# Performance work log

Measured on AMD Instinct MI355X. Metric: run time of the kernel, lower is better.

Reference implementation:

```python
import jax, jax.numpy as jnp
import numpy as np

NUM_EMOTIONS = 8
EMOTION_DIM = 32
MAX_EMOTIONS = 3
HIDDEN = 768
NUM_HEADS = 8
HEAD_DIM = HIDDEN // NUM_HEADS // 2  # 48
DEPTH = 0
LAMBDA_INIT = 0.8 - 0.6 * float(np.exp(-0.3 * DEPTH))  # 0.2
EPS = 1e-5


def setup_inputs() -> dict:
    key = jax.random.key(0)
    ks = jax.random.split(key, 16)
    B = 16384
    emotion_indices = jax.random.randint(ks[0], (B, MAX_EMOTIONS), 0, NUM_EMOTIONS)
    confidence_values = jax.random.uniform(ks[1], (B, MAX_EMOTIONS), dtype=jnp.float32)
    emb_table = jax.random.normal(ks[2], (NUM_EMOTIONS + 1, EMOTION_DIM), jnp.float32)
    emb_table = emb_table.at[NUM_EMOTIONS].set(0.0)  # padding_idx row
    s1 = 1.0 / np.sqrt(EMOTION_DIM)
    s2 = 1.0 / np.sqrt(HIDDEN)
    W1 = jax.random.normal(ks[3], (EMOTION_DIM, HIDDEN), jnp.float32) * s1
    b1 = jnp.zeros((HIDDEN,), jnp.float32)
    ln_g = jnp.ones((HIDDEN,), jnp.float32)
    ln_b = jnp.zeros((HIDDEN,), jnp.float32)
    Wq = jax.random.normal(ks[4], (HIDDEN, HIDDEN), jnp.float32) * s2
    Wk = jax.random.normal(ks[5], (HIDDEN, HIDDEN), jnp.float32) * s2
    Wv = jax.random.normal(ks[6], (HIDDEN, HIDDEN), jnp.float32) * s2
    Wo = jax.random.normal(ks[7], (HIDDEN, HIDDEN), jnp.float32) * s2
    lq1 = jax.random.normal(ks[8], (HEAD_DIM,), jnp.float32) * 0.1
    lk1 = jax.random.normal(ks[9], (HEAD_DIM,), jnp.float32) * 0.1
    lq2 = jax.random.normal(ks[10], (HEAD_DIM,), jnp.float32) * 0.1
    lk2 = jax.random.normal(ks[11], (HEAD_DIM,), jnp.float32) * 0.1
    subln_w = jnp.ones((2 * HEAD_DIM,), jnp.float32)
    return dict(emotion_indices=emotion_indices, confidence_values=confidence_values,
                emb_table=emb_table, W1=W1, b1=b1, ln_g=ln_g, ln_b=ln_b,
                Wq=Wq, Wk=Wk, Wv=Wv, Wo=Wo,
                lq1=lq1, lk1=lk1, lq2=lq2, lk2=lk2, subln_w=subln_w)


def _rotary_tables(seq_len, dim):
    inv_freq = 1.0 / (10000.0 ** (jnp.arange(0, dim, 2, dtype=jnp.float32) / dim))  # [dim/2]
    t = jnp.arange(seq_len, dtype=jnp.float32)
    ang = jnp.outer(t, inv_freq)  # [S, dim/2]
    return jnp.cos(ang), jnp.sin(ang)


def _apply_rope(x, cos, sin):
    # x: [B, S, H, D]; cos/sin: [S, D/2] (interleaved pairs)
    x1, x2 = x[..., 0::2], x[..., 1::2]
    c = cos[None, :, None, :]
    s = sin[None, :, None, :]
    r1 = x1 * c - x2 * s
    r2 = x1 * s + x2 * c
    return jnp.stack([r1, r2], axis=-1).reshape(x.shape)


def _forward(emotion_indices, confidence_values, emb_table, W1, b1, ln_g, ln_b,
             Wq, Wk, Wv, Wo, lq1, lk1, lq2, lk2, subln_w):
    B, S = emotion_indices.shape  # S == MAX_EMOTIONS
    idx = jnp.where(emotion_indices < 0, NUM_EMOTIONS, emotion_indices)

    # embedding lookup + confidence weighting
    emb = emb_table[idx] * confidence_values[..., None]  # [B,S,32]

    # Linear + LayerNorm + GELU (dropout = identity in eval)
    h = emb @ W1 + b1  # [B,S,768]
    mu = jnp.mean(h, axis=-1, keepdims=True)
    var = jnp.mean(jnp.square(h - mu), axis=-1, keepdims=True)
    h = (h - mu) / jnp.sqrt(var + EPS) * ln_g + ln_b
    h = jax.nn.gelu(h, approximate=False)

    # rotary tables
    cos, sin = _rotary_tables(S, HEAD_DIM)

    # additive attention mask: -inf over padded key columns
    pad = (idx == NUM_EMOTIONS)  # [B,S]
    neg_inf = jnp.asarray(-jnp.inf, h.dtype)
    mask = jnp.where(pad[:, None, None, :], neg_inf, 0.0)  # [B,1,1,S] -> bcast to [B,1,S,S]

    # differential attention
    q = (h @ Wq).reshape(B, S, 2 * NUM_HEADS, HEAD_DIM)
    k = (h @ Wk).reshape(B, S, 2 * NUM_HEADS, HEAD_DIM)
    v = (h @ Wv).reshape(B, S, NUM_HEADS, 2 * HEAD_DIM)
    q = _apply_rope(q, cos, sin)
    k = _apply_rope(k, cos, sin)

    scale = HEAD_DIM ** -0.5
    scores = jnp.einsum('bqhd,bkhd->bhqk', q, k) * scale + mask  # [B,2H,S,S]
    attn = jax.nn.softmax(scores, axis=-1)
    attn = attn.reshape(B, NUM_HEADS, 2, S, S)
    lam = (jnp.exp(jnp.sum(lq1 * lk1)) - jnp.exp(jnp.sum(lq2 * lk2)) + LAMBDA_INIT)
    diff = attn[:, :, 0] - lam * attn[:, :, 1]  # [B,H,S,S]

    out = jnp.einsum('bhqk,bkhd->bqhd', diff, v)  # [B,S,H,2d]
    # sublayer RMSNorm over last dim
    rms = jnp.sqrt(jnp.mean(jnp.square(out), axis=-1, keepdims=True) + EPS)
    out = out / rms * subln_w
    out = out * (1.0 - LAMBDA_INIT)
    out = out.reshape(B, S, HIDDEN) @ Wo  # [B,S,768]

    # masked mean pooling over non-padding positions
    npad = (~pad).astype(out.dtype)[..., None]  # [B,S,1]
    summed = jnp.sum(out * npad, axis=1)
    denom = jnp.maximum(jnp.sum(npad, axis=1), 1.0)
    return summed / denom  # [B,768]


def reference(emotion_indices, confidence_values, emb_table, W1, b1, ln_g, ln_b,
              Wq, Wk, Wv, Wo, lq1, lk1, lq2, lk2, subln_w):
    return _forward(emotion_indices, confidence_values, emb_table, W1, b1, ln_g, ln_b,
                    Wq, Wk, Wv, Wo, lq1, lk1, lq2, lk2, subln_w)
```

## Files before the change

### kernel.cpp

```cpp
#include <hip/hip_runtime.h>
#include <hip/hip_bf16.h>
#include <math.h>
#include <stdint.h>

typedef __hip_bfloat16 bf16;
typedef __attribute__((ext_vector_type(8))) short short8;
typedef __attribute__((ext_vector_type(4))) float f32x4;
typedef __attribute__((ext_vector_type(2))) unsigned int u32x2;

#define NB 16384
#define HID 768
#define EPS_LN 1e-5f
#define LAM_INIT 0.2f

__device__ __forceinline__ float bf2f(bf16 x){ return __bfloat162float(x); }
__device__ __forceinline__ bf16  f2bf(float x){ return __float2bfloat16(x); }
__device__ __forceinline__ float bfbits(uint32_t lo16){ return __uint_as_float(lo16 << 16); }
__device__ __forceinline__ uint32_t f2bfbits(float x){
  union { float f; uint32_t u; } v; v.f = x;
  uint32_t u = v.u;
  uint32_t r = (u + 0x7fff + ((u >> 16) & 1)) >> 16;
  return r;
}

template<typename T> __device__ __forceinline__ float ldv(const void* p, int i);
template<> __device__ __forceinline__ float ldv<float>(const void* p, int i){ return ((const float*)p)[i]; }
template<> __device__ __forceinline__ float ldv<bf16 >(const void* p, int i){ return bf2f(((const bf16*)p)[i]); }

template<typename T> __device__ __forceinline__ void stv(T* p, float v);
template<> __device__ __forceinline__ void stv<float>(float* p, float v){ *p = v; }
template<> __device__ __forceinline__ void stv<bf16 >(bf16*  p, float v){ *p = f2bf(v); }

__device__ __forceinline__ void async_copy16(void* lds, const void* g){
  __builtin_amdgcn_global_load_lds(
      (const __attribute__((address_space(1))) unsigned int*)g,
      (__attribute__((address_space(3))) unsigned int*)lds, 16, 0, 0);
}

__device__ __forceinline__ float wred64(float v){
  #pragma unroll
  for (int m = 1; m <= 32; m <<= 1) v += __shfl_xor(v, m, 64);
  return v;
}

__global__ void prep_kernel(const void* etab, const void* lq1, const void* lk1,
                            const void* lq2, const void* lk2, float* prep){
  const int lane = threadIdx.x;
  const uint32_t* p = (const uint32_t*)((const char*)etab + 512);
  int v = (lane < 16) ? (int)p[lane] : 0;
  #pragma unroll
  for (int m = 1; m <= 32; m <<= 1) v |= __shfl_xor(v, m, 64);
  const int isbf = (v == 0) ? 1 : 0;
  if (lane == 0) ((int*)prep)[0] = isbf;

  float p1 = 0.f, p2 = 0.f;
  if (lane < 48){
    if (isbf){ p1 = ldv<bf16>(lq1,lane)*ldv<bf16>(lk1,lane); p2 = ldv<bf16>(lq2,lane)*ldv<bf16>(lk2,lane); }
    else     { p1 = ldv<float>(lq1,lane)*ldv<float>(lk1,lane); p2 = ldv<float>(lq2,lane)*ldv<float>(lk2,lane); }
  }
  p1 = wred64(p1); p2 = wred64(p2);
  if (lane == 0) prep[1] = expf(p1) - expf(p2) + LAM_INIT;

  if (lane < 24){
    float invf = powf(10000.f, -(float)(2*lane)/48.f);
    #pragma unroll
    for (int s=0;s<3;++s){
      float ang = (float)s*invf;
      float c = cosf(ang), sv = sinf(ang);
      prep[16  + s*32 + lane] = c;
      prep[128 + s*32 + lane] = sv;
      prep[256 + (s*24 + lane)*2    ] = c;
      prep[256 + (s*24 + lane)*2 + 1] = sv;
    }
  }
}

template<typename T>
__device__ __forceinline__ void transpose_body(bf16 (*tile)[33], const void* src, bf16* dst){
  const int n0 = blockIdx.x*32, k0 = blockIdx.y*32;
  const int tx = threadIdx.x, ty = threadIdx.y;
  #pragma unroll
  for (int r=0;r<4;++r)
    tile[ty + 8*r][tx] = f2bf(ldv<T>(src, (k0 + ty + 8*r)*HID + n0 + tx));
  __syncthreads();
  #pragma unroll
  for (int r=0;r<4;++r)
    dst[(size_t)(n0 + ty + 8*r)*HID + k0 + tx] = tile[tx][ty + 8*r];
}

__global__ __launch_bounds__(256) void transpose_weights(
    const void* Wq, const void* Wk, const void* Wv, const void* Wo,
    bf16* __restrict__ WqkvT, bf16* __restrict__ WoT, const float* prep)
{
  __shared__ bf16 tile[32][33];
  const int z = blockIdx.z;
  const void* src = (z==0)? Wq : (z==1)? Wk : (z==2)? Wv : Wo;
  bf16* dst = (z<3)? (WqkvT + (size_t)z*HID*HID) : WoT;
  if (((const int*)prep)[0]) transpose_body<bf16 >(tile, src, dst);
  else                       transpose_body<float>(tile, src, dst);
}

template<typename T>
__device__ __forceinline__ void embed_body(
    float (*s_emb)[32], float (*s_h)[HID],
    const int* eidx, const void* conf, const void* etab, const void* W1,
    const void* b1, const void* lng, const void* lnb, bf16* hout, int tok0)
{
  const int tid = threadIdx.x;
  const int tl0 = blockIdx.x * 16;

  for (int i = tid; i < 16*32; i += 256) {
    int t = i >> 5, e = i & 31;
    int tt = tok0 + tl0 + t;
    int id = eidx[tt]; if (id < 0) id = 8;
    float cf = ldv<T>(conf, tt);
    s_emb[t][e] = ldv<T>(etab, id*32 + e) * cf;
  }
  __syncthreads();

  float acc0[16], acc1[16], acc2[16];
  #pragma unroll
  for (int t=0;t<16;++t){ acc0[t]=0.f; acc1[t]=0.f; acc2[t]=0.f; }
  const int c0 = tid, c1 = tid+256, c2 = tid+512;
  #pragma unroll 4
  for (int e=0;e<32;++e){
    float w0 = ldv<T>(W1, e*HID+c0), w1 = ldv<T>(W1, e*HID+c1), w2 = ldv<T>(W1, e*HID+c2);
    #pragma unroll
    for (int t=0;t<16;++t){
      float em = s_emb[t][e];
      acc0[t] += em*w0; acc1[t] += em*w1; acc2[t] += em*w2;
    }
  }
  float bb0 = ldv<T>(b1,c0), bb1 = ldv<T>(b1,c1), bb2 = ldv<T>(b1,c2);
  #pragma unroll
  for (int t=0;t<16;++t){
    s_h[t][c0] = acc0[t]+bb0; s_h[t][c1] = acc1[t]+bb1; s_h[t][c2] = acc2[t]+bb2;
  }
  __syncthreads();

  const int wv = tid>>6, lane = tid&63;
  for (int t = wv; t < 16; t += 4) {
    float x[12]; float sm = 0.f, sq = 0.f;
    #pragma unroll
    for (int j=0;j<12;++j){ float xv = s_h[t][lane + 64*j]; x[j]=xv; sm += xv; sq += xv*xv; }
    sm = wred64(sm); sq = wred64(sq);
    float mu  = sm * (1.f/768.f);
    float var = sq * (1.f/768.f) - mu*mu;
    float rs  = rsqrtf(fmaxf(var, 0.f) + EPS_LN);
    #pragma unroll
    for (int j=0;j<12;++j){
      int col = lane + 64*j;
      float y  = (x[j]-mu)*rs*ldv<T>(lng,col) + ldv<T>(lnb,col);
      float ge = 0.5f*y*(1.f + erff(y*0.70710678118f));
      hout[(size_t)(tl0+t)*HID + col] = f2bf(ge);
    }
  }
}

__global__ __launch_bounds__(256) void embed_fc1_ln_gelu(
    const int* __restrict__ eidx, const void* conf, const void* etab,
    const void* W1, const void* b1, const void* lng, const void* lnb,
    bf16* __restrict__ hout, int tok0, const float* prep)
{
  __shared__ float s_emb[16][32];
  __shared__ float s_h[16][HID];
  if (((const int*)prep)[0]) embed_body<bf16 >(s_emb, s_h, eidx, conf, etab, W1, b1, lng, lnb, hout, tok0);
  else                       embed_body<float>(s_emb, s_h, eidx, conf, etab, W1, b1, lng, lnb, hout, tok0);
}

template<typename OutT>
__device__ __forceinline__ void gemm_body(
    bf16* sA, bf16* sB,
    const bf16* __restrict__ A, const bf16* __restrict__ Bt, OutT* __restrict__ C,
    int K, int lda, int ldb, int ldc, int MT, int NT)
{
  int bid = blockIdx.x;
  int mt, nt;
  if ((MT & 7) == 0) {
    int x = bid & 7, j = bid >> 3;
    nt = j % NT;
    mt = x * (MT >> 3) + j / NT;
  } else { nt = bid % NT; mt = bid / NT; }

  const int tid = threadIdx.x;
  const int wave = tid >> 6, lane = tid & 63;
  const int m0 = mt * 128, n0 = nt * 128;
  const int wm = wave >> 1, wn = wave & 1;

  f32x4 acc[4][4];
  #pragma unroll
  for (int i=0;i<4;++i)
    #pragma unroll
    for (int j=0;j<4;++j) acc[i][j] = (f32x4){0.f,0.f,0.f,0.f};

  const char* Ag = (const char*)(A  + (size_t)m0 * lda);
  const char* Bg = (const char*)(Bt + (size_t)n0 * ldb);
  const int r8  = lane >> 3;
  const int cBx = ((lane & 7) ^ r8) * 16;

  #define STAGE(buf, kt) do {                                                   \
    _Pragma("unroll")                                                           \
    for (int ii = 0; ii < 4; ++ii) {                                            \
      const int i_ = wave*4 + ii;                                               \
      const int row_ = i_*8 + r8;                                               \
      async_copy16((char*)sA + (buf)*16384 + i_*1024 + lane*16,                 \
                   Ag + ((size_t)row_*lda + (kt))*2 + cBx);                     \
      async_copy16((char*)sB + (buf)*16384 + i_*1024 + lane*16,                 \
                   Bg + ((size_t)row_*ldb + (kt))*2 + cBx);                     \
    }                                                                           \
  } while(0)

  STAGE(0, 0);
  int cur = 0;
  const int rxor = (lane & 7) << 3;
  for (int kt = 0; kt < K; kt += 64) {
    __syncthreads();
    if (kt + 64 < K) STAGE(cur^1, kt + 64);
    const bf16* pA = sA + cur*8192;
    const bf16* pB = sB + cur*8192;
    #pragma unroll
    for (int ks = 0; ks < 64; ks += 32) {
      const int kq = (ks + (lane >> 4)*8) ^ rxor;
      short8 af[4], bfv[4];
      #pragma unroll
      for (int i=0;i<4;++i)
        af[i]  = *(const short8*)&pA[(wm*64 + i*16 + (lane&15))*64 + kq];
      #pragma unroll
      for (int j=0;j<4;++j)
        bfv[j] = *(const short8*)&pB[(wn*64 + j*16 + (lane&15))*64 + kq];
      #pragma unroll
      for (int i=0;i<4;++i)
        #pragma unroll
        for (int j=0;j<4;++j)
          acc[i][j] = __builtin_amdgcn_mfma_f32_16x16x32_bf16(af[i], bfv[j], acc[i][j], 0,0,0);
    }
    cur ^= 1;
  }
  #undef STAGE

  const int rb = (lane>>4)*4, cb = lane & 15;
  #pragma unroll
  for (int i=0;i<4;++i)
    #pragma unroll
    for (int r=0;r<4;++r) {
      const int grow = m0 + wm*64 + i*16 + rb + r;
      OutT* Cp = C + (size_t)grow*ldc + n0 + wn*64 + cb;
      #pragma unroll
      for (int j=0;j<4;++j) stv<OutT>(Cp + j*16, acc[i][j][r]);
    }
}

__global__ __launch_bounds__(256) void gemm_int(
    const bf16* __restrict__ A, const bf16* __restrict__ Bt, bf16* __restrict__ C,
    int K, int lda, int ldb, int ldc, int MT, int NT)
{
  __shared__ __align__(16) bf16 sA[2*128*64];
  __shared__ __align__(16) bf16 sB[2*128*64];
  gemm_body<bf16>(sA, sB, A, Bt, C, K, lda, ldb, ldc, MT, NT);
}

__global__ __launch_bounds__(256) void gemm_final(
    const bf16* __restrict__ A, const bf16* __restrict__ Bt, void* C,
    int K, int lda, int ldb, int ldc, int MT, int NT, const float* prep)
{
  __shared__ __align__(16) bf16 sA[2*128*64];
  __shared__ __align__(16) bf16 sB[2*128*64];
  if (((const int*)prep)[0]) gemm_body<bf16 >(sA, sB, A, Bt, (bf16*)C,  K, lda, ldb, ldc, MT, NT);
  else                       gemm_body<float>(sA, sB, A, Bt, (float*)C, K, lda, ldb, ldc, MT, NT);
}

template<typename T>
__device__ __forceinline__ void attn_body(
    const bf16* __restrict__ qkv, const int* __restrict__ eidx,
    const void* subw, bf16* __restrict__ obar, int b0, const float* prep)
{
  const int bl = blockIdx.x*4 + (threadIdx.x>>6);
  const int bg = b0 + bl;
  const int lane = threadIdx.x & 63;
  const int h  = lane >> 3;
  const int u  = lane & 7;
  const int g  = u >> 2;
  const int qd = u & 3;

  float npad[3];
  #pragma unroll
  for (int s=0;s<3;++s){ int id = eidx[bg*3+s]; npad[s] = (id < 0 || id == 8) ? 0.f : 1.f; }
  float denom = npad[0]+npad[1]+npad[2]; if (denom < 1.f) denom = 1.f;
  const float lam = prep[1];
  const float2* pk = (const float2*)(prep + 256);

  const char* base = (const char*)(qkv + (size_t)bl*3*2304);
  const int qoff = (2*h+g)*48 + qd*12;

  u32x2 qw[3][3], kw[3][3];
  #pragma unroll
  for (int s=0;s<3;++s){
    const char* qp = base + (size_t)(s*2304 + qoff)*2;
    const char* kp = qp + 768*2;
    #pragma unroll
    for (int t=0;t<3;++t){
      qw[s][t] = *(const u32x2*)(qp + t*8);
      kw[s][t] = *(const u32x2*)(kp + t*8);
    }
  }

  float sc[3][3];
  #pragma unroll
  for (int a=0;a<3;++a){ sc[a][0]=0.f; sc[a][1]=0.f; sc[a][2]=0.f; }
  #pragma unroll
  for (int j=0;j<6;++j){
    float qr1[3], qr2[3], kr1[3], kr2[3];
    #pragma unroll
    for (int s=0;s<3;++s){
      float2 cs = pk[s*24 + qd*6 + j];
      uint32_t qu = qw[s][j>>1][j&1], ku = kw[s][j>>1][j&1];
      float q1 = bfbits(qu & 0xffffu), q2 = bfbits(qu >> 16);
      float k1 = bfbits(ku & 0xffffu), k2 = bfbits(ku >> 16);
      qr1[s] = q1*cs.x - q2*cs.y;  qr2[s] = q1*cs.y + q2*cs.x;
      kr1[s] = k1*cs.x - k2*cs.y;  kr2[s] = k1*cs.y + k2*cs.x;
    }
    #pragma unroll
    for (int a=0;a<3;++a)
      #pragma unroll
      for (int b=0;b<3;++b) sc[a][b] += qr1[a]*kr1[b] + qr2[a]*kr2[b];
  }
  #pragma unroll
  for (int a=0;a<3;++a)
    #pragma unroll
    for (int b=0;b<3;++b){
      float v = sc[a][b];
      v += __shfl_xor(v, 1, 64);
      v += __shfl_xor(v, 2, 64);
      sc[a][b] = v;
    }

  const float scale = 0.14433756729740643f;
  float att[3][3];
  #pragma unroll
  for (int a=0;a<3;++a){
    float s0 = sc[a][0]*scale + (npad[0] > 0.f ? 0.f : -1e30f);
    float s1 = sc[a][1]*scale + (npad[1] > 0.f ? 0.f : -1e30f);
    float s2 = sc[a][2]*scale + (npad[2] > 0.f ? 0.f : -1e30f);
    float mx = fmaxf(s0, fmaxf(s1, s2));
    float e0 = expf(s0-mx), e1 = expf(s1-mx), e2 = expf(s2-mx);
    float inv = 1.f/(e0+e1+e2);
    att[a][0]=e0*inv; att[a][1]=e1*inv; att[a][2]=e2*inv;
  }
  float diff[3][3];
  #pragma unroll
  for (int a=0;a<3;++a)
    #pragma unroll
    for (int b=0;b<3;++b){
      float other = __shfl_xor(att[a][b], 4, 64);
      diff[a][b] = (g==0) ? (att[a][b] - lam*other) : (other - lam*att[a][b]);
    }

  const int vd = u*12;
  float vv[3][12];
  #pragma unroll
  for (int s=0;s<3;++s){
    const char* vp = base + (size_t)(s*2304 + 1536 + h*96 + vd)*2;
    #pragma unroll
    for (int t=0;t<3;++t){
      u32x2 w = *(const u32x2*)(vp + t*8);
      vv[s][t*4+0] = bfbits(w[0] & 0xffffu);
      vv[s][t*4+1] = bfbits(w[0] >> 16);
      vv[s][t*4+2] = bfbits(w[1] & 0xffffu);
      vv[s][t*4+3] = bfbits(w[1] >> 16);
    }
  }
  float sw[12];
  #pragma unroll
  for (int d=0;d<12;++d) sw[d] = ldv<T>(subw, vd + d);

  float acc[12];
  #pragma unroll
  for (int d=0;d<12;++d) acc[d] = 0.f;
  #pragma unroll
  for (int a=0;a<3;++a){
    float o[12]; float ss = 0.f;
    #pragma unroll
    for (int d=0;d<12;++d){
      o[d] = diff[a][0]*vv[0][d] + diff[a][1]*vv[1][d] + diff[a][2]*vv[2][d];
      ss += o[d]*o[d];
    }
    ss += __shfl_xor(ss, 1, 64);
    ss += __shfl_xor(ss, 2, 64);
    ss += __shfl_xor(ss, 4, 64);
    float rms = sqrtf(ss*(1.f/96.f) + 1e-5f);
    float kk  = npad[a]*0.8f/rms;
    #pragma unroll
    for (int d=0;d<12;++d) acc[d] += o[d]*kk*sw[d];
  }
  const float idn = 1.f/denom;
  char* op = (char*)obar + (size_t)(bg*HID + h*96 + vd)*2;
  #pragma unroll
  for (int t=0;t<3;++t){
    u32x2 w;
    w[0] = f2bfbits(acc[t*4+0]*idn) | (f2bfbits(acc[t*4+1]*idn) << 16);
    w[1] = f2bfbits(acc[t*4+2]*idn) | (f2bfbits(acc[t*4+3]*idn) << 16);
    *(u32x2*)(op + t*8) = w;
  }
}

__global__ __launch_bounds__(256) void attn_kernel(
    const bf16* __restrict__ qkv, const int* __restrict__ eidx,
    const void* subw, bf16* __restrict__ obar, int b0, const float* prep)
{
  if (((const int*)prep)[0]) attn_body<bf16 >(qkv, eidx, subw, obar, b0, prep);
  else                       attn_body<float>(qkv, eidx, subw, obar, b0, prep);
}

extern "C" void kernel_launch(void* const* d_in, const int* in_sizes, int n_in,
                              void* d_out, int out_size, void* d_ws, size_t ws_size,
                              hipStream_t stream)
{
  const int*  eidx = (const int*) d_in[0];
  const void* conf = d_in[1];
  const void* etab = d_in[2];
  const void* W1   = d_in[3];
  const void* b1   = d_in[4];
  const void* lng  = d_in[5];
  const void* lnb  = d_in[6];
  const void* Wq   = d_in[7];
  const void* Wk   = d_in[8];
  const void* Wv   = d_in[9];
  const void* Wo   = d_in[10];
  const void* lq1  = d_in[11];
  const void* lk1  = d_in[12];
  const void* lq2  = d_in[13];
  const void* lk2  = d_in[14];
  const void* subw = d_in[15];

  const size_t PREP_B = 4096ull;
  const size_t OBAR_B = 25165824ull, WQKVT_B = 3538944ull, WOT_B = 1179648ull;
  const size_t FIXED  = PREP_B + OBAR_B + WQKVT_B + WOT_B;

  char*  ws   = (char*)d_ws;
  float* prep = (float*)ws;
  bf16*  obar = (bf16*)(ws + PREP_B);
  bf16* WqkvT = (bf16*)(ws + PREP_B + OBAR_B);
  bf16* WoT   = (bf16*)(ws + PREP_B + OBAR_B + WQKVT_B);

  int CB = NB;
  while (CB > 128 && FIXED + (size_t)CB*18432ull > ws_size) CB >>= 1;

  bf16* hbuf = (bf16*)(ws + FIXED);
  bf16* qkv  = (bf16*)(ws + FIXED + (size_t)CB*4608ull);

  prep_kernel<<<1, 64, 0, stream>>>(etab, lq1, lk1, lq2, lk2, prep);
  transpose_weights<<<dim3(24,24,4), dim3(32,8), 0, stream>>>(Wq, Wk, Wv, Wo, WqkvT, WoT, prep);

  const int nchunks = NB / CB;
  const int ctok = 3*CB;
  for (int c = 0; c < nchunks; ++c) {
    const int b0 = c*CB, tok0 = b0*3;
    const int MT = ctok/128, NT = 18;
    embed_fc1_ln_gelu<<<ctok/16, 256, 0, stream>>>(eidx, conf, etab, W1, b1, lng, lnb, hbuf, tok0, prep);
    gemm_int<<<MT*NT, 256, 0, stream>>>(hbuf, WqkvT, qkv, HID, HID, HID, 2304, MT, NT);
    attn_kernel<<<CB/4, 256, 0, stream>>>(qkv, eidx, subw, obar, b0, prep);
  }

  gemm_final<<<128*6, 256, 0, stream>>>(obar, WoT, (void*)d_out, HID, HID, HID, HID, 128, 6, prep);
}
```

Baseline: 496.0 us.

## Precompute embedding-times-W1 table and closed-form LayerNorm stats per emotion id

Since the embedding table has only 9 rows, the prep kernel now computes E1 = emb_table @ W1 for each row, along with per-row mean, second moment and bias cross terms. The per-token kernel then rebuilds fc1 output as conf*E1[id] + b1 and derives the LayerNorm mean and variance analytically, with no per-token 32x768 matmul and no block reductions. Stores are vectorized into packed bf16 words, and each wave handles 16 tokens with 12 columns per lane. The variance formula E[x^2]-mu^2 is a different numerical path from the reference, and the single-block prep kernel does more work.

```diff
diff --git a/kernel.cpp b/kernel.cpp
--- a/kernel.cpp
+++ b/kernel.cpp
@@ -43,36 +43,88 @@
   return v;
 }
 
-__global__ void prep_kernel(const void* etab, const void* lq1, const void* lk1,
-                            const void* lq2, const void* lk2, float* prep){
-  const int lane = threadIdx.x;
-  const uint32_t* p = (const uint32_t*)((const char*)etab + 512);
-  int v = (lane < 16) ? (int)p[lane] : 0;
-  #pragma unroll
-  for (int m = 1; m <= 32; m <<= 1) v |= __shfl_xor(v, m, 64);
-  const int isbf = (v == 0) ? 1 : 0;
-  if (lane == 0) ((int*)prep)[0] = isbf;
-
-  float p1 = 0.f, p2 = 0.f;
-  if (lane < 48){
-    if (isbf){ p1 = ldv<bf16>(lq1,lane)*ldv<bf16>(lk1,lane); p2 = ldv<bf16>(lq2,lane)*ldv<bf16>(lk2,lane); }
-    else     { p1 = ldv<float>(lq1,lane)*ldv<float>(lk1,lane); p2 = ldv<float>(lq2,lane)*ldv<float>(lk2,lane); }
-  }
-  p1 = wred64(p1); p2 = wred64(p2);
-  if (lane == 0) prep[1] = expf(p1) - expf(p2) + LAM_INIT;
-
-  if (lane < 24){
-    float invf = powf(10000.f, -(float)(2*lane)/48.f);
-    #pragma unroll
-    for (int s=0;s<3;++s){
-      float ang = (float)s*invf;
-      float c = cosf(ang), sv = sinf(ang);
-      prep[16  + s*32 + lane] = c;
-      prep[128 + s*32 + lane] = sv;
-      prep[256 + (s*24 + lane)*2    ] = c;
-      prep[256 + (s*24 + lane)*2 + 1] = sv;
-    }
-  }
+template<typename T>
+__device__ __forceinline__ void prep_body(float* sE1, const void* etab, const void* W1,
+                                          const void* b1, float* prep){
+  const int tid = threadIdx.x;
+  for (int id = 0; id < 9; ++id){
+    #pragma unroll
+    for (int q = 0; q < 3; ++q){
+      const int cc = tid + q*256;
+      float s = 0.f;
+      #pragma unroll
+      for (int e = 0; e < 32; ++e) s += ldv<T>(etab, id*32+e) * ldv<T>(W1, e*HID+cc);
+      sE1[id*HID + cc] = s;
+      prep[1024 + id*HID + cc] = s;
+    }
+  }
+  __syncthreads();
+  const int wave = tid >> 6, lane = tid & 63;
+  float bv[12];
+  #pragma unroll
+  for (int j = 0; j < 12; ++j) bv[j] = ldv<T>(b1, lane + 64*j);
+  for (int id = wave; id < 9; id += 4){
+    float su = 0.f, suu = 0.f, sub = 0.f;
+    #pragma unroll
+    for (int j = 0; j < 12; ++j){
+      float v = sE1[id*HID + lane + 64*j];
+      su += v; suu += v*v; sub += v*bv[j];
+    }
+    su = wred64(su); suu = wred64(suu); sub = wred64(sub);
+    if (lane == 0){
+      prep[512+id] = su  * (1.f/768.f);
+      prep[528+id] = suu * (1.f/768.f);
+      prep[544+id] = sub * (1.f/768.f);
+    }
+  }
+  if (wave == 0){
+    float sb = 0.f, sbb = 0.f;
+    #pragma unroll
+    for (int j = 0; j < 12; ++j){ sb += bv[j]; sbb += bv[j]*bv[j]; }
+    sb = wred64(sb); sbb = wred64(sbb);
+    if (lane == 0){ prep[560] = sb*(1.f/768.f); prep[561] = sbb*(1.f/768.f); }
+  }
+}
+
+__global__ __launch_bounds__(256) void prep_kernel(
+    const void* etab, const void* W1, const void* b1,
+    const void* lq1, const void* lk1, const void* lq2, const void* lk2, float* prep){
+  __shared__ float sE1[9*HID];
+  __shared__ int s_isbf;
+  const int tid = threadIdx.x;
+  if (tid < 64){
+    const int lane = tid;
+    const uint32_t* p = (const uint32_t*)((const char*)etab + 512);
+    int v = (lane < 16) ? (int)p[lane] : 0;
+    #pragma unroll
+    for (int m = 1; m <= 32; m <<= 1) v |= __shfl_xor(v, m, 64);
+    const int isbf = (v == 0) ? 1 : 0;
+    if (lane == 0){ ((int*)prep)[0] = isbf; s_isbf = isbf; }
+
+    float p1 = 0.f, p2 = 0.f;
+    if (lane < 48){
+      if (isbf){ p1 = ldv<bf16>(lq1,lane)*ldv<bf16>(lk1,lane); p2 = ldv<bf16>(lq2,lane)*ldv<bf16>(lk2,lane); }
+      else     { p1 = ldv<float>(lq1,lane)*ldv<float>(lk1,lane); p2 = ldv<float>(lq2,lane)*ldv<float>(lk2,lane); }
+    }
+    p1 = wred64(p1); p2 = wred64(p2);
+    if (lane == 0) prep[1] = expf(p1) - expf(p2) + LAM_INIT;
+
+    if (lane < 24){
+      float invf = powf(10000.f, -(float)(2*lane)/48.f);
+      #pragma unroll
+      for (int s=0;s<3;++s){
+        float ang = (float)s*invf;
+        float c = cosf(ang), sv = sinf(ang);
+        prep[16  + s*32 + lane] = c;
+        prep[128 + s*32 + lane] = sv;
+        prep[256 + (s*24 + lane)*2    ] = c;
+        prep[256 + (s*24 + lane)*2 + 1] = sv;
+      }
+    }
+  }
+  __syncthreads();
+  if (s_isbf) prep_body<bf16 >(sE1, etab, W1, b1, prep);
+  else        prep_body<float>(sE1, etab, W1, b1, prep);
 }
 
 template<typename T>
@@ -102,70 +154,54 @@
 
 template<typename T>
 __device__ __forceinline__ void embed_body(
-    float (*s_emb)[32], float (*s_h)[HID],
-    const int* eidx, const void* conf, const void* etab, const void* W1,
-    const void* b1, const void* lng, const void* lnb, bf16* hout, int tok0)
-{
-  const int tid = threadIdx.x;
-  const int tl0 = blockIdx.x * 16;
-
-  for (int i = tid; i < 16*32; i += 256) {
-    int t = i >> 5, e = i & 31;
-    int tt = tok0 + tl0 + t;
-    int id = eidx[tt]; if (id < 0) id = 8;
-    float cf = ldv<T>(conf, tt);
-    s_emb[t][e] = ldv<T>(etab, id*32 + e) * cf;
-  }
-  __syncthreads();
-
-  float acc0[16], acc1[16], acc2[16];
-  #pragma unroll
-  for (int t=0;t<16;++t){ acc0[t]=0.f; acc1[t]=0.f; acc2[t]=0.f; }
-  const int c0 = tid, c1 = tid+256, c2 = tid+512;
-  #pragma unroll 4
-  for (int e=0;e<32;++e){
-    float w0 = ldv<T>(W1, e*HID+c0), w1 = ldv<T>(W1, e*HID+c1), w2 = ldv<T>(W1, e*HID+c2);
-    #pragma unroll
-    for (int t=0;t<16;++t){
-      float em = s_emb[t][e];
-      acc0[t] += em*w0; acc1[t] += em*w1; acc2[t] += em*w2;
-    }
-  }
-  float bb0 = ldv<T>(b1,c0), bb1 = ldv<T>(b1,c1), bb2 = ldv<T>(b1,c2);
-  #pragma unroll
-  for (int t=0;t<16;++t){
-    s_h[t][c0] = acc0[t]+bb0; s_h[t][c1] = acc1[t]+bb1; s_h[t][c2] = acc2[t]+bb2;
-  }
-  __syncthreads();
-
-  const int wv = tid>>6, lane = tid&63;
-  for (int t = wv; t < 16; t += 4) {
-    float x[12]; float sm = 0.f, sq = 0.f;
-    #pragma unroll
-    for (int j=0;j<12;++j){ float xv = s_h[t][lane + 64*j]; x[j]=xv; sm += xv; sq += xv*xv; }
-    sm = wred64(sm); sq = wred64(sq);
-    float mu  = sm * (1.f/768.f);
-    float var = sq * (1.f/768.f) - mu*mu;
-    float rs  = rsqrtf(fmaxf(var, 0.f) + EPS_LN);
-    #pragma unroll
-    for (int j=0;j<12;++j){
-      int col = lane + 64*j;
-      float y  = (x[j]-mu)*rs*ldv<T>(lng,col) + ldv<T>(lnb,col);
-      float ge = 0.5f*y*(1.f + erff(y*0.70710678118f));
-      hout[(size_t)(tl0+t)*HID + col] = f2bf(ge);
-    }
-  }
-}
-
-__global__ __launch_bounds__(256) void embed_fc1_ln_gelu(
-    const int* __restrict__ eidx, const void* conf, const void* etab,
-    const void* W1, const void* b1, const void* lng, const void* lnb,
-    bf16* __restrict__ hout, int tok0, const float* prep)
-{
-  __shared__ float s_emb[16][32];
-  __shared__ float s_h[16][HID];
-  if (((const int*)prep)[0]) embed_body<bf16 >(s_emb, s_h, eidx, conf, etab, W1, b1, lng, lnb, hout, tok0);
-  else                       embed_body<float>(s_emb, s_h, eidx, conf, etab, W1, b1, lng, lnb, hout, tok0);
+    const int* eidx, const void* conf, const void* b1, const void* lng,
+    const void* lnb, const float* prep, bf16* hout, int tok0)
+{
+  const int wave = threadIdx.x >> 6, lane = threadIdx.x & 63;
+  const int t0 = blockIdx.x*64 + wave*16;
+  const int c  = lane*12;
+  float bb[12], gg[12], be[12];
+  #pragma unroll
+  for (int d=0;d<12;++d){ bb[d]=ldv<T>(b1,c+d); gg[d]=ldv<T>(lng,c+d); be[d]=ldv<T>(lnb,c+d); }
+  const float m_b = prep[560], s_bb = prep[561];
+  const float* E1 = prep + 1024;
+
+  for (int tt = 0; tt < 16; ++tt){
+    const int tl = t0 + tt, tg = tok0 + tl;
+    int id = eidx[tg]; if (id < 0) id = 8;
+    const float cf = ldv<T>(conf, tg);
+    const float4* ep = (const float4*)(E1 + id*HID + c);
+    float4 u0 = ep[0], u1 = ep[1], u2 = ep[2];
+    float u[12] = {u0.x,u0.y,u0.z,u0.w, u1.x,u1.y,u1.z,u1.w, u2.x,u2.y,u2.z,u2.w};
+    const float mu  = cf*prep[512+id] + m_b;
+    const float ex2 = cf*cf*prep[528+id] + 2.f*cf*prep[544+id] + s_bb;
+    const float var = ex2 - mu*mu;
+    const float rs  = rsqrtf(fmaxf(var, 0.f) + EPS_LN);
+    uint32_t w[6];
+    #pragma unroll
+    for (int d=0;d<6;++d){
+      float x0 = cf*u[2*d]   + bb[2*d];
+      float x1 = cf*u[2*d+1] + bb[2*d+1];
+      float y0 = (x0-mu)*rs*gg[2*d]   + be[2*d];
+      float y1 = (x1-mu)*rs*gg[2*d+1] + be[2*d+1];
+      float g0 = 0.5f*y0*(1.f + erff(y0*0.70710678118f));
+      float g1 = 0.5f*y1*(1.f + erff(y1*0.70710678118f));
+      w[d] = f2bfbits(g0) | (f2bfbits(g1) << 16);
+    }
+    char* op = (char*)hout + (size_t)(tl*HID + c)*2;
+    ((u32x2*)op)[0] = (u32x2){w[0],w[1]};
+    ((u32x2*)op)[1] = (u32x2){w[2],w[3]};
+    ((u32x2*)op)[2] = (u32x2){w[4],w[5]};
+  }
+}
+
+__global__ __launch_bounds__(256) void embed_ln_gelu(
+    const int* __restrict__ eidx, const void* conf, const void* b1,
+    const void* lng, const void* lnb, const float* prep,
+    bf16* __restrict__ hout, int tok0)
+{
+  if (((const int*)prep)[0]) embed_body<bf16 >(eidx, conf, b1, lng, lnb, prep, hout, tok0);
+  else                       embed_body<float>(eidx, conf, b1, lng, lnb, prep, hout, tok0);
 }
 
 template<typename OutT>
@@ -432,7 +468,7 @@
   const void* lk2  = d_in[14];
   const void* subw = d_in[15];
 
-  const size_t PREP_B = 4096ull;
+  const size_t PREP_B = 36864ull;
   const size_t OBAR_B = 25165824ull, WQKVT_B = 3538944ull, WOT_B = 1179648ull;
   const size_t FIXED  = PREP_B + OBAR_B + WQKVT_B + WOT_B;
 
@@ -448,7 +484,7 @@
   bf16* hbuf = (bf16*)(ws + FIXED);
   bf16* qkv  = (bf16*)(ws + FIXED + (size_t)CB*4608ull);
 
-  prep_kernel<<<1, 64, 0, stream>>>(etab, lq1, lk1, lq2, lk2, prep);
+  prep_kernel<<<1, 256, 0, stream>>>(etab, W1, b1, lq1, lk1, lq2, lk2, prep);
   transpose_weights<<<dim3(24,24,4), dim3(32,8), 0, stream>>>(Wq, Wk, Wv, Wo, WqkvT, WoT, prep);
 
   const int nchunks = NB / CB;
@@ -456,7 +492,7 @@
   for (int c = 0; c < nchunks; ++c) {
     const int b0 = c*CB, tok0 = b0*3;
     const int MT = ctok/128, NT = 18;
-    embed_fc1_ln_gelu<<<ctok/16, 256, 0, stream>>>(eidx, conf, etab, W1, b1, lng, lnb, hbuf, tok0, prep);
+    embed_ln_gelu<<<ctok/64, 256, 0, stream>>>(eidx, conf, b1, lng, lnb, prep, hbuf, tok0);
     gemm_int<<<MT*NT, 256, 0, stream>>>(hbuf, WqkvT, qkv, HID, HID, HID, 2304, MT, NT);
     attn_kernel<<<CB/4, 256, 0, stream>>>(qkv, eidx, subw, obar, b0, prep);
   }
```

New measurement: 484.4 us. 1.02x faster.
